# Optimization experiments

Hardware: AMD Instinct MI355X
Metric: run time of the kernel (lower is better)

## Reference

```python
import jax, jax.numpy as jnp
import numpy as np
import math

B, S, D, H, DH = 1, 2048, 2048, 16, 64  # batch, seq, d_model, n_heads, d_head
LAMBDA_INIT = 0.8
EPS = 1e-5


def setup_inputs() -> dict:
    key = jax.random.key(0)
    ks = jax.random.split(key, 10)
    w_scale = 0.02
    inner = 2 * DH * H  # == D here
    return {
        "x": jax.random.normal(ks[0], (B, S, D), dtype=jnp.float32),
        "Wq": jax.random.normal(ks[1], (D, inner), dtype=jnp.float32) * w_scale,
        "Wk": jax.random.normal(ks[2], (D, inner), dtype=jnp.float32) * w_scale,
        "Wv": jax.random.normal(ks[3], (D, inner), dtype=jnp.float32) * w_scale,
        "Wo": jax.random.normal(ks[4], (inner, D), dtype=jnp.float32) * w_scale,
        "lambda_q1": jax.random.normal(ks[5], (DH,), dtype=jnp.float32) * 0.1,
        "lambda_k1": jax.random.normal(ks[6], (DH,), dtype=jnp.float32) * 0.1,
        "lambda_q2": jax.random.normal(ks[7], (DH,), dtype=jnp.float32) * 0.1,
        "lambda_k2": jax.random.normal(ks[8], (DH,), dtype=jnp.float32) * 0.1,
        "gn_weight": jnp.ones((inner,), dtype=jnp.float32),
        "gn_bias": jnp.zeros((inner,), dtype=jnp.float32),
    }


def reference(x, Wq, Wk, Wv, Wo, lambda_q1, lambda_k1, lambda_q2, lambda_k2,
              gn_weight, gn_bias):
    b, s, _ = x.shape
    dh = lambda_q1.shape[0]
    h = Wq.shape[1] // (2 * dh)
    scale = 1.0 / math.sqrt(dh)

    q = (x @ Wq).reshape(b, s, h, 2, dh)
    k = (x @ Wk).reshape(b, s, h, 2, dh)
    v = (x @ Wv).reshape(b, s, h, 2 * dh)

    # [B,H,S,dh]
    q1 = jnp.swapaxes(q[..., 0, :], 1, 2)
    q2 = jnp.swapaxes(q[..., 1, :], 1, 2)
    k1 = jnp.swapaxes(k[..., 0, :], 1, 2)
    k2 = jnp.swapaxes(k[..., 1, :], 1, 2)
    vh = jnp.swapaxes(v, 1, 2)  # [B,H,S,2*dh]

    score1 = jnp.einsum("bhsd,bhtd->bhst", q1, k1) * scale
    score2 = jnp.einsum("bhsd,bhtd->bhst", q2, k2) * scale
    attn1 = jax.nn.softmax(score1, axis=-1)
    attn2 = jax.nn.softmax(score2, axis=-1)

    lam = (jnp.exp(jnp.sum(lambda_q1 * lambda_k1))
           - jnp.exp(jnp.sum(lambda_q2 * lambda_k2)) + LAMBDA_INIT)

    out = jnp.einsum("bhst,bhtd->bhsd", attn1 - lam * attn2, vh)  # [B,H,S,2dh]
    out = jnp.swapaxes(out, 1, 2)  # [B,S,H,2dh]

    # GroupNorm: n_heads groups over the channel dim, per token
    mu = jnp.mean(out, axis=-1, keepdims=True)
    var = jnp.var(out, axis=-1, keepdims=True)
    out = (out - mu) * jax.lax.rsqrt(var + EPS)
    gw = gn_weight.reshape(h, 2 * dh)
    gb = gn_bias.reshape(h, 2 * dh)
    out = out * gw + gb

    out = out * (1.0 - LAMBDA_INIT)
    return out.reshape(b, s, -1) @ Wo
```

## Files before the change

### kernel.cpp

```cpp
#include <hip/hip_runtime.h>
#include <hip/hip_bf16.h>

typedef unsigned short u16;
typedef __attribute__((ext_vector_type(8))) short short8;
typedef __attribute__((ext_vector_type(4))) short short4v;
typedef __attribute__((ext_vector_type(4))) float f32x4;

#define S_DIM 2048
#define D_DIM 2048
#define H_NUM 16
#define DH_NUM 64

#if __has_builtin(__builtin_amdgcn_exp2f)
#define EXP2(x) __builtin_amdgcn_exp2f(x)
#else
#define EXP2(x) exp2f(x)
#endif

__device__ __forceinline__ u16 f2bf(float f) {
    union { float f; unsigned u; } x; x.f = f;
    unsigned r = x.u + 0x7fff + ((x.u >> 16) & 1);
    return (u16)(r >> 16);
}

__device__ __forceinline__ unsigned pk_bf16(float a, float b) {
    union { __hip_bfloat162 h; unsigned u; } cv;
    float2 t; t.x = a; t.y = b;
    cv.h = __float22bfloat162_rn(t);
    return cv.u;
}

__device__ __forceinline__ void lane_swap32(unsigned &a, unsigned &b) {
    asm("v_permlane32_swap_b32 %0, %1" : "+v"(a), "+v"(b));
}
__device__ __forceinline__ void lane_swap16(unsigned &a, unsigned &b) {
    asm("v_permlane16_swap_b32 %0, %1" : "+v"(a), "+v"(b));
}

__device__ __forceinline__ void gload16(const void* g, void* l) {
    __builtin_amdgcn_global_load_lds(
        (const __attribute__((address_space(1))) unsigned int*)g,
        (__attribute__((address_space(3))) unsigned int*)l, 16, 0, 0);
}

__device__ __forceinline__ void transpose_body(const float* __restrict__ src,
                                               u16* __restrict__ dst,
                                               int tx, int ty, int t)
{
    __shared__ float tile[64][65];
    const int r0 = ty * 64, c0 = tx * 64;
#pragma unroll
    for (int p = 0; p < 4; ++p) {
        int r = p * 16 + (t >> 4), c = (t & 15) * 4;
        float4 v = *(const float4*)&src[(long)(r0 + r) * D_DIM + c0 + c];
        tile[r][c] = v.x; tile[r][c + 1] = v.y;
        tile[r][c + 2] = v.z; tile[r][c + 3] = v.w;
    }
    __syncthreads();
#pragma unroll
    for (int p = 0; p < 2; ++p) {
        int ch = t + p * 256;
        int i = ch >> 3, j0 = (ch & 7) * 8;
        short8 o;
#pragma unroll
        for (int jj = 0; jj < 8; ++jj)
            o[jj] = (short)f2bf(tile[j0 + jj][i]);
        *(short8*)&dst[(long)(c0 + i) * D_DIM + r0 + j0] = o;
    }
}

__global__ __launch_bounds__(256)
void transpose_fast(const float* __restrict__ src, u16* __restrict__ dst)
{
    transpose_body(src, dst, blockIdx.x, blockIdx.y, threadIdx.x);
}

__global__ __launch_bounds__(256)
void prep4(const float* __restrict__ x,
           const float* __restrict__ Wq, const float* __restrict__ Wk,
           const float* __restrict__ Wv, const float* __restrict__ Wo,
           u16* __restrict__ XB, u16* T0, u16* T1, u16* T2, u16* T3)
{
    const int z = blockIdx.z, t = threadIdx.x, bx = blockIdx.x;
    if (z == 0) {
        long i0 = ((long)bx * 256 + t) * 16;
        short8 o0, o1;
#pragma unroll
        for (int j = 0; j < 2; ++j) {
            float4 a = *(const float4*)&x[i0 + j * 8];
            float4 b = *(const float4*)&x[i0 + j * 8 + 4];
            short8& o = j ? o1 : o0;
            o[0] = (short)f2bf(a.x); o[1] = (short)f2bf(a.y);
            o[2] = (short)f2bf(a.z); o[3] = (short)f2bf(a.w);
            o[4] = (short)f2bf(b.x); o[5] = (short)f2bf(b.y);
            o[6] = (short)f2bf(b.z); o[7] = (short)f2bf(b.w);
        }
        *(short8*)&XB[i0] = o0;
        *(short8*)&XB[i0 + 8] = o1;
    } else {
        const float* src = (z == 1) ? Wq : (z == 2) ? Wk : (z == 3) ? Wv : Wo;
        u16* dst         = (z == 1) ? T0 : (z == 2) ? T1 : (z == 3) ? T2 : T3;
        transpose_body(src, dst, bx & 31, bx >> 5, t);
    }
}

__global__ __launch_bounds__(256)
void cvt_bf16(const float* __restrict__ src, u16* __restrict__ dst)
{
    int i = (blockIdx.x * 256 + threadIdx.x) * 4;
    float4 v = *(const float4*)(src + i);
    ushort4 o;
    o.x = f2bf(v.x); o.y = f2bf(v.y); o.z = f2bf(v.z); o.w = f2bf(v.w);
    *(ushort4*)(dst + i) = o;
}

__global__ __launch_bounds__(256, 2)
void gemm128(const u16* __restrict__ A,
             const u16* B0, const u16* B1, const u16* B2,
             u16* C0, u16* C1, u16* C2, int zbase)
{
    const int Kd = D_DIM, N = D_DIM, M = S_DIM;

    int bx, by, z;
    if (gridDim.z == 3) {
        int b  = blockIdx.x + (blockIdx.y << 4) + (blockIdx.z << 8);
        int nb = (b & 7) * 96 + (b >> 3);
        z = nb % 3;
        int t = nb / 3;
        bx = t & 15; by = t >> 4;
    } else {
        bx = blockIdx.x; by = blockIdx.y; z = zbase;
    }

    const u16* Bt = (z == 0) ? B0 : (z == 1) ? B1 : B2;
    u16* C        = (z == 0) ? C0 : (z == 1) ? C1 : C2;

    __shared__ __attribute__((aligned(16))) u16 As[2][128 * 64];
    __shared__ __attribute__((aligned(16))) u16 Bs[2][128 * 64];

    const int tid = threadIdx.x, lane = tid & 63, wave = tid >> 6;
    const int bm = bx * 128, bn = by * 128;

    const int grow = lane >> 3;
    const int gcol = ((lane & 7) ^ grow) * 8;

    const int wr = (wave >> 1) * 64, wc = (wave & 1) * 64;
    const int fr = lane & 15, fq = lane >> 4;
    const int swz = fr & 7;

    f32x4 acc[4][4];
    for (int i = 0; i < 4; ++i)
        for (int j = 0; j < 4; ++j) { f32x4 zz = {0.f,0.f,0.f,0.f}; acc[i][j] = zz; }

    auto stage = [&](int k0, int b) {
#pragma unroll
        for (int g = 0; g < 4; ++g) {
            int r = wave * 32 + g * 8;
            gload16(A + (long)(bm + r + grow) * Kd + k0 + gcol, &As[b][r * 64]);
            gload16(Bt + (long)(bn + r + grow) * Kd + k0 + gcol, &Bs[b][r * 64]);
        }
    };

    stage(0, 0);
    int p = 0;
    const int NT = Kd / 64;

    for (int t = 0; t < NT; ++t) {
        __syncthreads();
        if (t + 1 < NT) stage((t + 1) * 64, p ^ 1);

#pragma unroll
        for (int ks = 0; ks < 2; ++ks) {
            const int slot = ((fq + ks * 4) ^ swz) * 8;
            short8 af[4], bf[4];
#pragma unroll
            for (int i = 0; i < 4; ++i) {
                af[i] = *(const short8*)&As[p][(wr + i * 16 + fr) * 64 + slot];
                bf[i] = *(const short8*)&Bs[p][(wc + i * 16 + fr) * 64 + slot];
            }
            if (z == 2) {
#pragma unroll
                for (int i = 0; i < 4; ++i)
#pragma unroll
                    for (int j = 0; j < 4; ++j)
                        acc[i][j] = __builtin_amdgcn_mfma_f32_16x16x32_bf16(bf[j], af[i], acc[i][j], 0, 0, 0);
            } else {
#pragma unroll
                for (int i = 0; i < 4; ++i)
#pragma unroll
                    for (int j = 0; j < 4; ++j)
                        acc[i][j] = __builtin_amdgcn_mfma_f32_16x16x32_bf16(af[i], bf[j], acc[i][j], 0, 0, 0);
            }
        }
        p ^= 1;
    }

    if (z == 2) {
#pragma unroll
        for (int i = 0; i < 4; ++i) {
            int tok = bm + wr + i * 16 + fr;
#pragma unroll
            for (int j = 0; j < 4; ++j) {
                int ch = bn + wc + j * 16 + fq * 4;
#pragma unroll
                for (int r = 0; r < 4; ++r)
                    C[(long)(ch + r) * M + tok] = f2bf(acc[i][j][r]);
            }
        }
    } else {
        const float sc = (z == 0) ? 0.125f * 1.44269504f : 1.0f;
#pragma unroll
        for (int i = 0; i < 4; ++i) {
            int row = bm + wr + i * 16 + fq * 4;
#pragma unroll
            for (int j = 0; j < 4; ++j) {
                int col = bn + wc + j * 16 + fr;
#pragma unroll
                for (int r = 0; r < 4; ++r)
                    C[(long)(row + r) * N + col] = f2bf(acc[i][j][r] * sc);
            }
        }
    }
}

__global__ __launch_bounds__(256, 2)
void gemm_out(const u16* __restrict__ A, const u16* __restrict__ Bt,
              float* __restrict__ C)
{
    const int Kd = D_DIM, N = D_DIM;

    __shared__ __attribute__((aligned(16))) u16 As[2][128 * 64];
    __shared__ __attribute__((aligned(16))) u16 Bs[2][128 * 64];

    const int b0 = blockIdx.x + (blockIdx.y << 4);
    const int nb = (b0 & 7) * 32 + (b0 >> 3);
    const int bm = (nb & 15) * 128, bn = (nb >> 4) * 128;

    const int tid = threadIdx.x, lane = tid & 63, wave = tid >> 6;

    const int grow = lane >> 3;
    const int gcol = ((lane & 7) ^ grow) * 8;

    const int wr = (wave >> 1) * 64, wc = (wave & 1) * 64;
    const int fr = lane & 15, fq = lane >> 4;
    const int swz = fr & 7;

    f32x4 acc[4][4];
    for (int i = 0; i < 4; ++i)
        for (int j = 0; j < 4; ++j) { f32x4 zz = {0.f,0.f,0.f,0.f}; acc[i][j] = zz; }

    auto stage = [&](int k0, int b) {
#pragma unroll
        for (int g = 0; g < 4; ++g) {
            int r = wave * 32 + g * 8;
            gload16(A + (long)(bm + r + grow) * Kd + k0 + gcol, &As[b][r * 64]);
            gload16(Bt + (long)(bn + r + grow) * Kd + k0 + gcol, &Bs[b][r * 64]);
        }
    };

    stage(0, 0);
    int p = 0;
    const int NT = Kd / 64;

    for (int t = 0; t < NT; ++t) {
        __syncthreads();
        if (t + 1 < NT) stage((t + 1) * 64, p ^ 1);

#pragma unroll
        for (int ks = 0; ks < 2; ++ks) {
            const int slot = ((fq + ks * 4) ^ swz) * 8;
            short8 af[4], bf[4];
#pragma unroll
            for (int i = 0; i < 4; ++i) {
                af[i] = *(const short8*)&As[p][(wr + i * 16 + fr) * 64 + slot];
                bf[i] = *(const short8*)&Bs[p][(wc + i * 16 + fr) * 64 + slot];
            }
#pragma unroll
            for (int i = 0; i < 4; ++i)
#pragma unroll
                for (int j = 0; j < 4; ++j)
                    acc[i][j] = __builtin_amdgcn_mfma_f32_16x16x32_bf16(af[i], bf[j], acc[i][j], 0, 0, 0);
        }
        p ^= 1;
    }

#pragma unroll
    for (int i = 0; i < 4; ++i) {
        int row = bm + wr + i * 16 + fq * 4;
#pragma unroll
        for (int j = 0; j < 4; ++j) {
            int col = bn + wc + j * 16 + fr;
#pragma unroll
            for (int r = 0; r < 4; ++r)
                C[(long)(row + r) * N + col] = acc[i][j][r];
        }
    }
}

__global__ __launch_bounds__(256, 2)
void diff_attn(const u16* __restrict__ Qm, const u16* __restrict__ Km,
               const u16* __restrict__ Vt,
               const float* __restrict__ lq1, const float* __restrict__ lk1,
               const float* __restrict__ lq2, const float* __restrict__ lk2,
               const float* __restrict__ gw, const float* __restrict__ gb,
               u16* __restrict__ Y)
{
    __shared__ __attribute__((aligned(16))) u16 K1s[2][64 * 64];
    __shared__ __attribute__((aligned(16))) u16 K2s[2][64 * 64];
    __shared__ __attribute__((aligned(16))) u16 Vts[2][128 * 64];

    const int tid = threadIdx.x, lane = tid & 63, wave = tid >> 6;
    const int h = blockIdx.y;
    const int q0 = blockIdx.x * 64 + wave * 16;
    const int fr = lane & 15, qq = lane >> 4;
    const int fsw = fr & 7;

    const int grow = lane >> 3;
    const int gcol = ((lane & 7) ^ grow) * 8;

    float d1 = 0.f, d2 = 0.f;
    for (int i = 0; i < DH_NUM; ++i) {
        d1 += lq1[i] * lk1[i];
        d2 += lq2[i] * lk2[i];
    }
    const float lam = __expf(d1) - __expf(d2) + 0.8f;

    short8 q1f[2], q2f[2];
    {
        const u16* qb = Qm + (long)(q0 + fr) * D_DIM + h * 128;
        q1f[0] = *(const short8*)(qb + qq * 8);
        q1f[1] = *(const short8*)(qb + 32 + qq * 8);
        q2f[0] = *(const short8*)(qb + 64 + qq * 8);
        q2f[1] = *(const short8*)(qb + 96 + qq * 8);
    }

    f32x4 a1[8], a2[8];
    for (int n = 0; n < 8; ++n) { f32x4 zz = {0.f,0.f,0.f,0.f}; a1[n] = zz; a2[n] = zz; }
    float ls1 = 0.f, ls2 = 0.f;

    auto stage = [&](int kb, int b) {
        const long kbase = (long)(kb * 64) * D_DIM + h * 128;
#pragma unroll
        for (int g = 0; g < 2; ++g) {
            int r = wave * 16 + g * 8;
            gload16(Km + kbase + (long)(r + grow) * D_DIM + gcol,      &K1s[b][r * 64]);
            gload16(Km + kbase + (long)(r + grow) * D_DIM + 64 + gcol, &K2s[b][r * 64]);
        }
#pragma unroll
        for (int g = 0; g < 4; ++g) {
            int c = wave * 32 + g * 8;
            gload16(Vt + (long)(h * 128 + c + grow) * S_DIM + kb * 64 + gcol,
                    &Vts[b][c * 64]);
        }
    };

    stage(0, 0);
    int p = 0;

    for (int kb = 0; kb < S_DIM / 64; ++kb) {
        __syncthreads();
        const bool more = (kb + 1 < S_DIM / 64);
        if (more) stage(kb + 1, p ^ 1);

#pragma unroll
        for (int jj = 0; jj < 2; ++jj) {
            short8 k1r[2][2], k2r[2][2];
#pragma unroll
            for (int jh = 0; jh < 2; ++jh) {
                const int j = jj * 2 + jh;
#pragma unroll
                for (int ks = 0; ks < 2; ++ks) {
                    const int slot = ((ks * 4 + qq) ^ fsw) * 8;
                    k1r[jh][ks] = *(const short8*)&K1s[p][(j * 16 + fr) * 64 + slot];
                    k2r[jh][ks] = *(const short8*)&K2s[p][(j * 16 + fr) * 64 + slot];
                }
            }
            const int slotV = ((jj * 4 + qq) ^ fsw) * 8;
            short8 vf[8];
#pragma unroll
            for (int n = 0; n < 8; ++n)
                vf[n] = *(const short8*)&Vts[p][(n * 16 + fr) * 64 + slotV];

            unsigned u1[2][2], u2[2][2];
#pragma unroll
            for (int jh = 0; jh < 2; ++jh) {
                f32x4 s1 = {0.f,0.f,0.f,0.f}, s2 = {0.f,0.f,0.f,0.f};
#pragma unroll
                for (int ks = 0; ks < 2; ++ks) {
                    s1 = __builtin_amdgcn_mfma_f32_16x16x32_bf16(k1r[jh][ks], q1f[ks], s1, 0, 0, 0);
                    s2 = __builtin_amdgcn_mfma_f32_16x16x32_bf16(k2r[jh][ks], q2f[ks], s2, 0, 0, 0);
                }
                float e1[4], e2[4];
#pragma unroll
                for (int r = 0; r < 4; ++r) {
                    e1[r] = EXP2(s1[r]);
                    e2[r] = EXP2(s2[r]);
                    ls1 += e1[r]; ls2 += e2[r];
                }
                u1[jh][0] = pk_bf16(e1[0], e1[1]); u1[jh][1] = pk_bf16(e1[2], e1[3]);
                u2[jh][0] = pk_bf16(e2[0], e2[1]); u2[jh][1] = pk_bf16(e2[2], e2[3]);
            }

            union { short8 s; unsigned u[4]; } F1, F2;
            {
                unsigned x = u1[0][0], y = u1[1][0];
                lane_swap32(x, y); lane_swap16(x, y);
                F1.u[0] = x; F1.u[2] = y;
            }
            {
                unsigned x = u1[0][1], y = u1[1][1];
                lane_swap32(x, y); lane_swap16(x, y);
                F1.u[1] = x; F1.u[3] = y;
            }
            {
                unsigned x = u2[0][0], y = u2[1][0];
                lane_swap32(x, y); lane_swap16(x, y);
                F2.u[0] = x; F2.u[2] = y;
            }
            {
                unsigned x = u2[0][1], y = u2[1][1];
                lane_swap32(x, y); lane_swap16(x, y);
                F2.u[1] = x; F2.u[3] = y;
            }

            __builtin_amdgcn_s_setprio(1);
#pragma unroll
            for (int n = 0; n < 8; ++n) {
                a1[n] = __builtin_amdgcn_mfma_f32_16x16x32_bf16(vf[n], F1.s, a1[n], 0, 0, 0);
                a2[n] = __builtin_amdgcn_mfma_f32_16x16x32_bf16(vf[n], F2.s, a2[n], 0, 0, 0);
            }
            __builtin_amdgcn_s_setprio(0);
        }

        p ^= 1;
    }

    float L1 = ls1, L2 = ls2;
    L1 += __shfl_xor(L1, 16, 64); L1 += __shfl_xor(L1, 32, 64);
    L2 += __shfl_xor(L2, 16, 64); L2 += __shfl_xor(L2, 32, 64);
    const float i1 = 1.f / L1, i2 = lam / L2;

    float o[8][4], sum = 0.f, sq = 0.f;
#pragma unroll
    for (int n = 0; n < 8; ++n)
#pragma unroll
        for (int r = 0; r < 4; ++r) {
            float v = a1[n][r] * i1 - a2[n][r] * i2;
            o[n][r] = v; sum += v; sq += v * v;
        }
    sum += __shfl_xor(sum, 16, 64); sum += __shfl_xor(sum, 32, 64);
    sq  += __shfl_xor(sq, 16, 64);  sq  += __shfl_xor(sq, 32, 64);
    const float mean = sum * (1.f / 128.f);
    const float var = sq * (1.f / 128.f) - mean * mean;
    const float inv = rsqrtf(var + 1e-5f);

    const long yrow = (long)(q0 + fr) * D_DIM + h * 128;
#pragma unroll
    for (int n = 0; n < 8; ++n) {
        float4 g4 = *(const float4*)&gw[h * 128 + n * 16 + qq * 4];
        float4 b4 = *(const float4*)&gb[h * 128 + n * 16 + qq * 4];
        ushort4 st;
        st.x = f2bf(((o[n][0] - mean) * inv * g4.x + b4.x) * 0.2f);
        st.y = f2bf(((o[n][1] - mean) * inv * g4.y + b4.y) * 0.2f);
        st.z = f2bf(((o[n][2] - mean) * inv * g4.z + b4.z) * 0.2f);
        st.w = f2bf(((o[n][3] - mean) * inv * g4.w + b4.w) * 0.2f);
        *(ushort4*)&Y[yrow + n * 16 + qq * 4] = st;
    }
}

extern "C" void kernel_launch(void* const* d_in, const int* in_sizes, int n_in,
                              void* d_out, int out_size, void* d_ws, size_t ws_size,
                              hipStream_t stream)
{
    const float* x   = (const float*)d_in[0];
    const float* Wq  = (const float*)d_in[1];
    const float* Wk  = (const float*)d_in[2];
    const float* Wv  = (const float*)d_in[3];
    const float* Wo  = (const float*)d_in[4];
    const float* lq1 = (const float*)d_in[5];
    const float* lk1 = (const float*)d_in[6];
    const float* lq2 = (const float*)d_in[7];
    const float* lk2 = (const float*)d_in[8];
    const float* gw  = (const float*)d_in[9];
    const float* gb  = (const float*)d_in[10];

    char* ws = (char*)d_ws;
    const size_t SEG = (size_t)D_DIM * D_DIM * sizeof(u16);
    const dim3 tgrid(32, 32), agrid(32, 16), ogrid(16, 16);

    if (ws_size >= 8 * SEG) {
        u16* XB  = (u16*)(ws + 0 * SEG);
        u16* WTq = (u16*)(ws + 1 * SEG);
        u16* WTk = (u16*)(ws + 2 * SEG);
        u16* WTv = (u16*)(ws + 3 * SEG);
        u16* Qb  = (u16*)(ws + 4 * SEG);
        u16* Kb  = (u16*)(ws + 5 * SEG);
        u16* Vt  = (u16*)(ws + 6 * SEG);
        u16* WTo = (u16*)(ws + 7 * SEG);
        u16* Yb  = WTk;

        prep4<<<dim3(1024, 1, 5), 256, 0, stream>>>(x, Wq, Wk, Wv, Wo,
                                                    XB, WTq, WTk, WTv, WTo);
        gemm128<<<dim3(16, 16, 3), 256, 0, stream>>>(XB, WTq, WTk, WTv,
                                                     Qb, Kb, Vt, 0);
        diff_attn<<<agrid, 256, 0, stream>>>(Qb, Kb, Vt, lq1, lk1, lq2, lk2,
                                             gw, gb, Yb);
        gemm_out<<<ogrid, 256, 0, stream>>>(Yb, WTo, (float*)d_out);
    } else if (ws_size >= 7 * SEG) {
        u16* XB  = (u16*)(ws + 0 * SEG);
        u16* WTq = (u16*)(ws + 1 * SEG);
        u16* WTk = (u16*)(ws + 2 * SEG);
        u16* WTv = (u16*)(ws + 3 * SEG);
        u16* Qb  = (u16*)(ws + 4 * SEG);
        u16* Kb  = (u16*)(ws + 5 * SEG);
        u16* Vt  = (u16*)(ws + 6 * SEG);
        u16* WTo = WTq;
        u16* Yb  = WTk;

        prep4<<<dim3(1024, 1, 4), 256, 0, stream>>>(x, Wq, Wk, Wv, Wo,
                                                    XB, WTq, WTk, WTv, WTq);
        gemm128<<<dim3(16, 16, 3), 256, 0, stream>>>(XB, WTq, WTk, WTv,
                                                     Qb, Kb, Vt, 0);
        transpose_fast<<<tgrid, 256, 0, stream>>>(Wo, WTo);
        diff_attn<<<agrid, 256, 0, stream>>>(Qb, Kb, Vt, lq1, lk1, lq2, lk2,
                                             gw, gb, Yb);
        gemm_out<<<ogrid, 256, 0, stream>>>(Yb, WTo, (float*)d_out);
    } else {
        u16* XB = (u16*)(ws + 0 * SEG);
        u16* WT = (u16*)(ws + 1 * SEG);
        u16* Qb = (u16*)(ws + 2 * SEG);
        u16* Kb = (u16*)(ws + 3 * SEG);
        u16* Vt = (u16*)(ws + 4 * SEG);

        cvt_bf16<<<4096, 256, 0, stream>>>(x, XB);
        transpose_fast<<<tgrid, 256, 0, stream>>>(Wq, WT);
        gemm128<<<dim3(16, 16, 1), 256, 0, stream>>>(XB, WT, WT, WT, Qb, Qb, Qb, 0);
        transpose_fast<<<tgrid, 256, 0, stream>>>(Wk, WT);
        gemm128<<<dim3(16, 16, 1), 256, 0, stream>>>(XB, WT, WT, WT, Kb, Kb, Kb, 1);
        transpose_fast<<<tgrid, 256, 0, stream>>>(Wv, WT);
        gemm128<<<dim3(16, 16, 1), 256, 0, stream>>>(XB, WT, WT, WT, Vt, Vt, Vt, 2);
        diff_attn<<<agrid, 256, 0, stream>>>(Qb, Kb, Vt, lq1, lk1, lq2, lk2,
                                             gw, gb, XB);
        transpose_fast<<<tgrid, 256, 0, stream>>>(Wo, WT);
        gemm_out<<<ogrid, 256, 0, stream>>>(XB, WT, (float*)d_out);
    }
}
```

Measured before the change: 305.6 us.

## Split-K the output GEMM and interleave LDS loads with MFMAs in attention

The output projection GEMM is split along K into two halves via a z grid dimension, doubling the block count to 512 so more of the many CUs are occupied. The second half writes to a float workspace buffer, and a new add_out kernel sums it into the output. In the attention kernel, K and V fragment loads from LDS move to just before their MFMAs instead of being preloaded into register arrays, which cuts register pressure. The cost is an extra 16MB fp32 partial write/read plus a kernel launch, and the later LDS loads may stall the MFMAs if the compiler cannot overlap them.

```diff
diff --git a/kernel.cpp b/kernel.cpp
--- a/kernel.cpp
+++ b/kernel.cpp
@@ -112,6 +112,16 @@
     ushort4 o;
     o.x = f2bf(v.x); o.y = f2bf(v.y); o.z = f2bf(v.z); o.w = f2bf(v.w);
     *(ushort4*)(dst + i) = o;
+}
+
+__global__ __launch_bounds__(256)
+void add_out(float* __restrict__ C, const float* __restrict__ P)
+{
+    int i = (blockIdx.x * 256 + threadIdx.x) * 4;
+    float4 c = *(const float4*)&C[i];
+    float4 p = *(const float4*)&P[i];
+    c.x += p.x; c.y += p.y; c.z += p.z; c.w += p.w;
+    *(float4*)&C[i] = c;
 }
 
 __global__ __launch_bounds__(256, 2)
@@ -225,16 +235,20 @@
 
 __global__ __launch_bounds__(256, 2)
 void gemm_out(const u16* __restrict__ A, const u16* __restrict__ Bt,
-              float* __restrict__ C)
+              float* __restrict__ C, float* __restrict__ P)
 {
     const int Kd = D_DIM, N = D_DIM;
 
     __shared__ __attribute__((aligned(16))) u16 As[2][128 * 64];
     __shared__ __attribute__((aligned(16))) u16 Bs[2][128 * 64];
 
-    const int b0 = blockIdx.x + (blockIdx.y << 4);
-    const int nb = (b0 & 7) * 32 + (b0 >> 3);
-    const int bm = (nb & 15) * 128, bn = (nb >> 4) * 128;
+    const int b0 = blockIdx.x + (blockIdx.y << 4) + (blockIdx.z << 8);
+    const int nb = (b0 & 7) * 64 + (b0 >> 3);
+    const int kz = nb >> 8;
+    const int t8 = nb & 255;
+    const int bm = (t8 & 15) * 128, bn = (t8 >> 4) * 128;
+    const int k0base = kz * (Kd / 2);
+    float* __restrict__ Cd = kz ? P : C;
 
     const int tid = threadIdx.x, lane = tid & 63, wave = tid >> 6;
 
@@ -258,13 +272,13 @@
         }
     };
 
-    stage(0, 0);
+    stage(k0base, 0);
     int p = 0;
-    const int NT = Kd / 64;
+    const int NT = Kd / 2 / 64;
 
     for (int t = 0; t < NT; ++t) {
         __syncthreads();
-        if (t + 1 < NT) stage((t + 1) * 64, p ^ 1);
+        if (t + 1 < NT) stage(k0base + (t + 1) * 64, p ^ 1);
 
 #pragma unroll
         for (int ks = 0; ks < 2; ++ks) {
@@ -292,7 +306,7 @@
             int col = bn + wc + j * 16 + fr;
 #pragma unroll
             for (int r = 0; r < 4; ++r)
-                C[(long)(row + r) * N + col] = acc[i][j][r];
+                Cd[(long)(row + r) * N + col] = acc[i][j][r];
         }
     }
 }
@@ -364,31 +378,18 @@
 
 #pragma unroll
         for (int jj = 0; jj < 2; ++jj) {
-            short8 k1r[2][2], k2r[2][2];
+            unsigned u1[2][2], u2[2][2];
 #pragma unroll
             for (int jh = 0; jh < 2; ++jh) {
                 const int j = jj * 2 + jh;
+                f32x4 s1 = {0.f,0.f,0.f,0.f}, s2 = {0.f,0.f,0.f,0.f};
 #pragma unroll
                 for (int ks = 0; ks < 2; ++ks) {
                     const int slot = ((ks * 4 + qq) ^ fsw) * 8;
-                    k1r[jh][ks] = *(const short8*)&K1s[p][(j * 16 + fr) * 64 + slot];
-                    k2r[jh][ks] = *(const short8*)&K2s[p][(j * 16 + fr) * 64 + slot];
-                }
-            }
-            const int slotV = ((jj * 4 + qq) ^ fsw) * 8;
-            short8 vf[8];
-#pragma unroll
-            for (int n = 0; n < 8; ++n)
-                vf[n] = *(const short8*)&Vts[p][(n * 16 + fr) * 64 + slotV];
-
-            unsigned u1[2][2], u2[2][2];
-#pragma unroll
-            for (int jh = 0; jh < 2; ++jh) {
-                f32x4 s1 = {0.f,0.f,0.f,0.f}, s2 = {0.f,0.f,0.f,0.f};
-#pragma unroll
-                for (int ks = 0; ks < 2; ++ks) {
-                    s1 = __builtin_amdgcn_mfma_f32_16x16x32_bf16(k1r[jh][ks], q1f[ks], s1, 0, 0, 0);
-                    s2 = __builtin_amdgcn_mfma_f32_16x16x32_bf16(k2r[jh][ks], q2f[ks], s2, 0, 0, 0);
+                    short8 k1 = *(const short8*)&K1s[p][(j * 16 + fr) * 64 + slot];
+                    short8 k2 = *(const short8*)&K2s[p][(j * 16 + fr) * 64 + slot];
+                    s1 = __builtin_amdgcn_mfma_f32_16x16x32_bf16(k1, q1f[ks], s1, 0, 0, 0);
+                    s2 = __builtin_amdgcn_mfma_f32_16x16x32_bf16(k2, q2f[ks], s2, 0, 0, 0);
                 }
                 float e1[4], e2[4];
 #pragma unroll
@@ -423,11 +424,13 @@
                 F2.u[1] = x; F2.u[3] = y;
             }
 
+            const int slotV = ((jj * 4 + qq) ^ fsw) * 8;
             __builtin_amdgcn_s_setprio(1);
 #pragma unroll
             for (int n = 0; n < 8; ++n) {
-                a1[n] = __builtin_amdgcn_mfma_f32_16x16x32_bf16(vf[n], F1.s, a1[n], 0, 0, 0);
-                a2[n] = __builtin_amdgcn_mfma_f32_16x16x32_bf16(vf[n], F2.s, a2[n], 0, 0, 0);
+                short8 vf = *(const short8*)&Vts[p][(n * 16 + fr) * 64 + slotV];
+                a1[n] = __builtin_amdgcn_mfma_f32_16x16x32_bf16(vf, F1.s, a1[n], 0, 0, 0);
+                a2[n] = __builtin_amdgcn_mfma_f32_16x16x32_bf16(vf, F2.s, a2[n], 0, 0, 0);
             }
             __builtin_amdgcn_s_setprio(0);
         }
@@ -486,7 +489,7 @@
 
     char* ws = (char*)d_ws;
     const size_t SEG = (size_t)D_DIM * D_DIM * sizeof(u16);
-    const dim3 tgrid(32, 32), agrid(32, 16), ogrid(16, 16);
+    const dim3 tgrid(32, 32), agrid(32, 16), ogrid(16, 16, 2);
 
     if (ws_size >= 8 * SEG) {
         u16* XB  = (u16*)(ws + 0 * SEG);
@@ -498,6 +501,7 @@
         u16* Vt  = (u16*)(ws + 6 * SEG);
         u16* WTo = (u16*)(ws + 7 * SEG);
         u16* Yb  = WTk;
+        float* P = (float*)(ws + 0 * SEG);
 
         prep4<<<dim3(1024, 1, 5), 256, 0, stream>>>(x, Wq, Wk, Wv, Wo,
                                                     XB, WTq, WTk, WTv, WTo);
@@ -505,7 +509,8 @@
                                                      Qb, Kb, Vt, 0);
         diff_attn<<<agrid, 256, 0, stream>>>(Qb, Kb, Vt, lq1, lk1, lq2, lk2,
                                              gw, gb, Yb);
-        gemm_out<<<ogrid, 256, 0, stream>>>(Yb, WTo, (float*)d_out);
+        gemm_out<<<ogrid, 256, 0, stream>>>(Yb, WTo, (float*)d_out, P);
+        add_out<<<4096, 256, 0, stream>>>((float*)d_out, P);
     } else if (ws_size >= 7 * SEG) {
         u16* XB  = (u16*)(ws + 0 * SEG);
         u16* WTq = (u16*)(ws + 1 * SEG);
@@ -514,8 +519,9 @@
         u16* Qb  = (u16*)(ws + 4 * SEG);
         u16* Kb  = (u16*)(ws + 5 * SEG);
         u16* Vt  = (u16*)(ws + 6 * SEG);
-        u16* WTo = WTq;
+        u16* WTo = WTv;
         u16* Yb  = WTk;
+        float* P = (float*)(ws + 0 * SEG);
 
         prep4<<<dim3(1024, 1, 4), 256, 0, stream>>>(x, Wq, Wk, Wv, Wo,
                                                     XB, WTq, WTk, WTv, WTq);
@@ -524,13 +530,15 @@
         transpose_fast<<<tgrid, 256, 0, stream>>>(Wo, WTo);
         diff_attn<<<agrid, 256, 0, stream>>>(Qb, Kb, Vt, lq1, lk1, lq2, lk2,
                                              gw, gb, Yb);
-        gemm_out<<<ogrid, 256, 0, stream>>>(Yb, WTo, (float*)d_out);
+        gemm_out<<<ogrid, 256, 0, stream>>>(Yb, WTo, (float*)d_out, P);
+        add_out<<<4096, 256, 0, stream>>>((float*)d_out, P);
     } else {
         u16* XB = (u16*)(ws + 0 * SEG);
         u16* WT = (u16*)(ws + 1 * SEG);
         u16* Qb = (u16*)(ws + 2 * SEG);
         u16* Kb = (u16*)(ws + 3 * SEG);
         u16* Vt = (u16*)(ws + 4 * SEG);
+        float* P = (float*)(ws + 2 * SEG);
 
         cvt_bf16<<<4096, 256, 0, stream>>>(x, XB);
         transpose_fast<<<tgrid, 256, 0, stream>>>(Wq, WT);
@@ -542,6 +550,7 @@
         diff_attn<<<agrid, 256, 0, stream>>>(Qb, Kb, Vt, lq1, lk1, lq2, lk2,
                                              gw, gb, XB);
         transpose_fast<<<tgrid, 256, 0, stream>>>(Wo, WT);
-        gemm_out<<<ogrid, 256, 0, stream>>>(XB, WT, (float*)d_out);
-    }
-}
+        gemm_out<<<ogrid, 256, 0, stream>>>(XB, WT, (float*)d_out, P);
+        add_out<<<4096, 256, 0, stream>>>((float*)d_out, P);
+    }
+}
```

New measurement: 299.1 us. 1.02x faster.
